# Optimization experiments

Hardware: AMD Instinct MI355X
Metric: run time of the kernel (lower is better)

## Reference

```python
import jax, jax.numpy as jnp
import numpy as np

# init hyperparameters (from init_kwargs)
KD = KH = KW = 3
SD = SH = SW = 1
PD = PH = PW = 1
DD = DH = DW = 1
GROUPS = 1
DG = 1  # deformable_groups
CIN, COUT = 32, 64


def setup_inputs() -> dict:
    key = jax.random.key(0)
    k1, k2, k3, k4, k5 = jax.random.split(key, 5)
    B, D, H, W = 2, 8, 48, 48
    K = KD * KH * KW
    x = jax.random.normal(k1, (B, CIN, D, H, W), dtype=jnp.float32)
    # 2 offset components (h, w) per deformable-group kernel tap
    offset = jax.random.normal(k2, (B, 2 * DG * K, D, H, W), dtype=jnp.float32)
    mask = jax.random.uniform(k3, (B, DG * K, D, H, W), dtype=jnp.float32)
    fan_in = CIN // GROUPS * K
    weight = jax.random.normal(k4, (COUT, CIN // GROUPS, KD, KH, KW), dtype=jnp.float32) / np.sqrt(fan_in)
    bias = jax.random.uniform(k5, (COUT,), dtype=jnp.float32, minval=-1.0, maxval=1.0) / np.sqrt(fan_in)
    return {"input": x, "offset": offset, "mask": mask, "weight": weight, "bias": bias}


def reference(input, offset, mask, weight, bias):
    x = input
    B, Cin, D, H, W = x.shape
    Cout = weight.shape[0]
    K = KD * KH * KW
    Do = (D + 2 * PD - DD * (KD - 1) - 1) // SD + 1
    Ho = (H + 2 * PH - DH * (KH - 1) - 1) // SH + 1
    Wo = (W + 2 * PW - DW * (KW - 1) - 1) // SW + 1
    Cg = Cin // DG

    kdi, khi, kwi = [a.reshape(-1) for a in jnp.meshgrid(
        jnp.arange(KD), jnp.arange(KH), jnp.arange(KW), indexing="ij")]
    # depth taps: regular (un-deformed) dilated grid -> exact integer index
    d_pos = kdi[:, None] * DD + jnp.arange(Do) * SD - PD           # [K, Do]
    valid_d = (d_pos >= 0) & (d_pos < D)
    d_idx = jnp.clip(d_pos, 0, D - 1)
    h_base = (khi[:, None] * DH + jnp.arange(Ho) * SH - PH).astype(x.dtype)  # [K, Ho]
    w_base = (kwi[:, None] * DW + jnp.arange(Wo) * SW - PW).astype(x.dtype)  # [K, Wo]

    off = offset.reshape(B, DG, K, 2, Do, Ho, Wo)
    m = mask.reshape(B, DG, K, Do, Ho, Wo)

    h = h_base[None, None, :, None, :, None] + off[:, :, :, 0]     # [B,DG,K,Do,Ho,Wo]
    w = w_base[None, None, :, None, None, :] + off[:, :, :, 1]
    h0f, w0f = jnp.floor(h), jnp.floor(w)
    lh, lw = h - h0f, w - w0f
    h0, w0 = h0f.astype(jnp.int32), w0f.astype(jnp.int32)
    h1, w1 = h0 + 1, w0 + 1

    vd = valid_d[None, None, :, :, None, None]
    inb_h = lambda hi: (hi >= 0) & (hi < H)
    inb_w = lambda wi: (wi >= 0) & (wi < W)

    xg = x.reshape(B, DG, Cg, D, H, W)

    def gather(hI, wI):
        hc = jnp.clip(hI, 0, H - 1)
        wc = jnp.clip(wI, 0, W - 1)
        def per(xi, hh, ww):  # xi [Cg,D,H,W]; hh,ww [K,Do,Ho,Wo]
            dfull = jnp.broadcast_to(d_idx[:, :, None, None], hh.shape)
            return xi[:, dfull, hh, ww]  # [Cg,K,Do,Ho,Wo]
        return jax.vmap(jax.vmap(per))(xg, hc, wc)  # [B,DG,Cg,K,Do,Ho,Wo]

    w00 = ((1 - lh) * (1 - lw) * (inb_h(h0) & inb_w(w0) & vd))[:, :, None]
    w01 = ((1 - lh) * lw * (inb_h(h0) & inb_w(w1) & vd))[:, :, None]
    w10 = (lh * (1 - lw) * (inb_h(h1) & inb_w(w0) & vd))[:, :, None]
    w11 = (lh * lw * (inb_h(h1) & inb_w(w1) & vd))[:, :, None]

    val = (gather(h0, w0) * w00 + gather(h0, w1) * w01 +
           gather(h1, w0) * w10 + gather(h1, w1) * w11)   # [B,DG,Cg,K,Do,Ho,Wo]

    sampled = (val * m[:, :, None]).reshape(B, Cin, K, Do, Ho, Wo)
    w2 = weight.reshape(Cout, Cin // GROUPS, K)  # groups == 1
    out = jnp.einsum("bckdhw,ock->bodhw", sampled, w2)
    return out + bias[None, :, None, None, None]
```

## Files before the change

kernel.cpp:

```cpp
#include <hip/hip_runtime.h>
#include <hip/hip_bf16.h>
#include <hip/hip_fp16.h>

#define BSZ 2
#define CIN 32
#define COUT 64
#define DD_ 8
#define HH_ 48
#define WW_ 48
#define KK 27
#define HWs (HH_*WW_)
#define DHW (DD_*HH_*WW_)
#define NT 768
#define NBLK (BSZ*DD_*HH_)

typedef __attribute__((ext_vector_type(8))) _Float16 half8;
typedef __attribute__((ext_vector_type(4))) float f32x4;

__global__ void prep(const float* __restrict__ x, const float* __restrict__ wsrc,
                     _Float16* __restrict__ xT, _Float16* __restrict__ wf) {
    __shared__ float tile[CIN][WW_];
    int blk = blockIdx.x;
    if (blk < NBLK) {
        int h = blk % HH_;
        int t0 = blk / HH_;
        int d = t0 % DD_;
        int b = t0 / DD_;
        int base = d * HWs + h * WW_;
        for (int e = threadIdx.x; e < CIN * WW_; e += 256) {
            int ci = e / WW_, w = e - ci * WW_;
            tile[ci][w] = x[(size_t)(b * CIN + ci) * DHW + base + w];
        }
        __syncthreads();
        for (int e = threadIdx.x; e < CIN * WW_; e += 256) {
            int w = e >> 5, ci = e & 31;
            xT[(size_t)(b * DHW + base + w) * CIN + ci] = (_Float16)tile[ci][w];
        }
    } else {
        int idx = (blk - NBLK) * 256 + threadIdx.x;
        if (idx < KK * 4 * 64 * 8) {
            int j = idx & 7, l = (idx >> 3) & 63, c = (idx >> 9) & 3, k = idx >> 11;
            int co = c * 16 + (l & 15), ci = (l >> 4) * 8 + j;
            wf[idx] = (_Float16)wsrc[(co * CIN + ci) * KK + k];
        }
    }
}

#define SPLAT8(H) {H, H, H, H, H, H, H, H}

template<int USE_XT>
__launch_bounds__(NT, 4)
__global__ void dcn3d(const float* __restrict__ x, const _Float16* __restrict__ xT,
                      const float* __restrict__ off, const float* __restrict__ msk,
                      const float* __restrict__ wsrc, const _Float16* __restrict__ wf,
                      const float* __restrict__ bias, float* __restrict__ out) {
    int blk = blockIdx.x;
    int h = blk % HH_;
    int t0 = blk / HH_;
    int d = t0 % DD_;
    int b = t0 / DD_;

    __shared__ half8 Sh[14 * 3 * 4 * 16];

    int tid = threadIdx.x;
    int lane = tid & 63;
    int wid = tid >> 6;
    int cstrip = wid & 3;
    int T = wid >> 2;
    int spb = d * HWs + h * WW_;

    const _Float16* xTb = xT + (size_t)b * DHW * CIN;
    const float* xb = x + (size_t)b * CIN * DHW;

#define PREP(HF, NK, KB)                                                        \
    int sp00_##HF = 0, sp01_##HF = 0, sp10_##HF = 0, sp11_##HF = 0;             \
    float f00_##HF = 0.f, f01_##HF = 0.f, f10_##HF = 0.f, f11_##HF = 0.f;       \
    if (tid < (NK) * 48) {                                                      \
        int kl = tid / 48;                                                      \
        int w = tid - kl * 48;                                                  \
        int k = (KB) + kl;                                                      \
        int kd = k / 9, kh2 = (k / 3) % 3, kw2 = k % 3;                         \
        int dpos = d + kd - 1;                                                  \
        bool vd = (dpos >= 0) && (dpos < DD_);                                  \
        int didx = min(max(dpos, 0), DD_ - 1);                                  \
        int rb = didx * HWs;                                                    \
        int sp = spb + w;                                                       \
        float oh = off[(b * (2 * KK) + 2 * k) * DHW + sp];                      \
        float ow = off[(b * (2 * KK) + 2 * k + 1) * DHW + sp];                  \
        float m  = msk[(b * KK + k) * DHW + sp];                                \
        float vm = vd ? m : 0.f;                                                \
        float hhf = (float)(kh2 + h - 1) + oh;                                  \
        float wwf = (float)(kw2 + w - 1) + ow;                                  \
        float h0f = floorf(hhf), w0f = floorf(wwf);                             \
        float lh = hhf - h0f, lw = wwf - w0f;                                   \
        int h0 = (int)h0f, w0 = (int)w0f, h1 = h0 + 1, w1 = w0 + 1;             \
        bool ih0 = (h0 >= 0) && (h0 < HH_), ih1 = (h1 >= 0) && (h1 < HH_);      \
        bool iw0 = (w0 >= 0) && (w0 < WW_), iw1 = (w1 >= 0) && (w1 < WW_);      \
        int h0c = min(max(h0, 0), HH_ - 1), h1c = min(max(h1, 0), HH_ - 1);     \
        int w0c = min(max(w0, 0), WW_ - 1), w1c = min(max(w1, 0), WW_ - 1);     \
        f00_##HF = (ih0 && iw0) ? (1.f - lh) * (1.f - lw) * vm : 0.f;           \
        f01_##HF = (ih0 && iw1) ? (1.f - lh) * lw * vm : 0.f;                   \
        f10_##HF = (ih1 && iw0) ? lh * (1.f - lw) * vm : 0.f;                   \
        f11_##HF = (ih1 && iw1) ? lh * lw * vm : 0.f;                           \
        sp00_##HF = rb + h0c * WW_ + w0c;                                       \
        sp01_##HF = rb + h0c * WW_ + w1c;                                       \
        sp10_##HF = rb + h1c * WW_ + w0c;                                       \
        sp11_##HF = rb + h1c * WW_ + w1c;                                       \
    }

    PREP(0, 14, 0)
    PREP(1, 13, 14)

#define SAMPLE(HF, NK)                                                          \
    if (tid < (NK) * 48) {                                                      \
        int kl = tid / 48;                                                      \
        int w = tid - kl * 48;                                                  \
        int sb = (kl * 3 + (w >> 4)) * 64 + (w & 15);                           \
        if (USE_XT) {                                                           \
            _Float16 e00 = (_Float16)f00_##HF, e01 = (_Float16)f01_##HF;        \
            _Float16 e10 = (_Float16)f10_##HF, e11 = (_Float16)f11_##HF;        \
            half8 v00 = SPLAT8(e00), v01 = SPLAT8(e01);                         \
            half8 v10 = SPLAT8(e10), v11 = SPLAT8(e11);                         \
            const half8* p00 = (const half8*)(xTb + ((size_t)sp00_##HF << 5));  \
            const half8* p01 = (const half8*)(xTb + ((size_t)sp01_##HF << 5));  \
            const half8* p10 = (const half8*)(xTb + ((size_t)sp10_##HF << 5));  \
            const half8* p11 = (const half8*)(xTb + ((size_t)sp11_##HF << 5));  \
            _Pragma("unroll")                                                   \
            for (int g = 0; g < 4; ++g)                                         \
                Sh[sb + g * 16] = p00[g] * v00 + p01[g] * v01                   \
                                + p10[g] * v10 + p11[g] * v11;                  \
        } else {                                                                \
            _Pragma("unroll")                                                   \
            for (int g = 0; g < 4; ++g) {                                       \
                half8 cv;                                                       \
                _Pragma("unroll")                                               \
                for (int j = 0; j < 8; ++j) {                                   \
                    const float* xp = xb + (size_t)(g * 8 + j) * DHW;           \
                    float v = f00_##HF * xp[sp00_##HF] + f01_##HF * xp[sp01_##HF] \
                            + f10_##HF * xp[sp10_##HF] + f11_##HF * xp[sp11_##HF]; \
                    cv[j] = (_Float16)v;                                        \
                }                                                               \
                Sh[sb + g * 16] = cv;                                           \
            }                                                                   \
        }                                                                       \
    }

    f32x4 acc = {0.f, 0.f, 0.f, 0.f};

#define GEMM(NK, KB)                                                            \
    _Pragma("unroll 7")                                                         \
    for (int kl = 0; kl < (NK); ++kl) {                                         \
        half8 a;                                                                \
        if (USE_XT) {                                                           \
            a = *(const half8*)(wf + ((((KB) + kl) * 4 + cstrip) * 64 + lane) * 8); \
        } else {                                                                \
            int co = cstrip * 16 + (lane & 15);                                 \
            int ci0 = (lane >> 4) * 8;                                          \
            _Pragma("unroll")                                                   \
            for (int j = 0; j < 8; ++j)                                         \
                a[j] = (_Float16)wsrc[(co * CIN + ci0 + j) * KK + (KB) + kl];   \
        }                                                                       \
        half8 bf = Sh[(kl * 3 + T) * 64 + (lane >> 4) * 16 + (lane & 15)];      \
        acc = __builtin_amdgcn_mfma_f32_16x16x32_f16(a, bf, acc, 0, 0, 0);      \
    }

    SAMPLE(0, 14)
    __syncthreads();
    GEMM(14, 0)
    __syncthreads();
    SAMPLE(1, 13)
    __syncthreads();
    GEMM(13, 14)

    int co0 = cstrip * 16 + (lane >> 4) * 4;
    int wcol = T * 16 + (lane & 15);
#pragma unroll
    for (int r = 0; r < 4; ++r)
        out[((b * COUT + co0 + r) * DD_ + d) * HWs + h * WW_ + wcol] = acc[r] + bias[co0 + r];

#undef PREP
#undef SAMPLE
#undef GEMM
}

extern "C" void kernel_launch(void* const* d_in, const int* in_sizes, int n_in,
                              void* d_out, int out_size, void* d_ws, size_t ws_size,
                              hipStream_t stream) {
    const float* x    = (const float*)d_in[0];
    const float* off  = (const float*)d_in[1];
    const float* msk  = (const float*)d_in[2];
    const float* w    = (const float*)d_in[3];
    const float* bias = (const float*)d_in[4];
    float* out = (float*)d_out;

    const size_t WF_BYTES = (size_t)KK * 4 * 64 * 8 * sizeof(_Float16);
    const size_t XT_OFF   = 131072;
    const size_t XT_BYTES = (size_t)BSZ * DHW * CIN * sizeof(_Float16);

    _Float16* wf = (_Float16*)d_ws;
    _Float16* xT = (_Float16*)((char*)d_ws + XT_OFF);
    int use = (ws_size >= XT_OFF + XT_BYTES && WF_BYTES <= XT_OFF) ? 1 : 0;

    if (use) {
        int wblocks = (KK * 4 * 64 * 8 + 255) / 256;
        prep<<<NBLK + wblocks, 256, 0, stream>>>(x, w, xT, wf);
        dcn3d<1><<<NBLK, NT, 0, stream>>>(x, xT, off, msk, w, wf, bias, out);
    } else {
        dcn3d<0><<<NBLK, NT, 0, stream>>>(x, xT, off, msk, w, wf, bias, out);
    }
}
```

Measured before the change: 43.50 us.

## Split kernel taps across three blocks with atomic accumulation into bias-initialized output

The main kernel now launches three times as many blocks, each covering a group of 9 of the 27 kernel taps for one output row. Partial results are combined with atomicAdd into an output buffer that a new kernel pre-fills with bias. The sampling loop is also rebalanced so each thread handles one 8-channel slice instead of all four, and the launch bound is raised to 6 blocks per CU. This is meant to increase parallelism and occupancy, at the cost of an extra launch, atomic traffic on the output, and a nondeterministic summation order.

```diff
diff --git a/kernel.cpp b/kernel.cpp
--- a/kernel.cpp
+++ b/kernel.cpp
@@ -1,5 +1,4 @@
 #include <hip/hip_runtime.h>
-#include <hip/hip_bf16.h>
 #include <hip/hip_fp16.h>
 
 #define BSZ 2
@@ -11,11 +10,21 @@
 #define KK 27
 #define HWs (HH_*WW_)
 #define DHW (DD_*HH_*WW_)
+#define NBLK (BSZ*DD_*HH_)
+#define KG 9
 #define NT 768
-#define NBLK (BSZ*DD_*HH_)
 
 typedef __attribute__((ext_vector_type(8))) _Float16 half8;
 typedef __attribute__((ext_vector_type(4))) float f32x4;
+
+__global__ void init_out(const float* __restrict__ bias, float* __restrict__ out) {
+    int o4 = blockIdx.x * 256 + threadIdx.x;
+    if (o4 >= BSZ * COUT * DHW / 4) return;
+    int o = o4 * 4;
+    float bv = bias[(o / DHW) & (COUT - 1)];
+    float4 v = {bv, bv, bv, bv};
+    *(float4*)(out + o) = v;
+}
 
 __global__ void prep(const float* __restrict__ x, const float* __restrict__ wsrc,
                      _Float16* __restrict__ xT, _Float16* __restrict__ wf) {
@@ -46,141 +55,119 @@
     }
 }
 
-#define SPLAT8(H) {H, H, H, H, H, H, H, H}
-
 template<int USE_XT>
-__launch_bounds__(NT, 4)
+__launch_bounds__(NT, 6)
 __global__ void dcn3d(const float* __restrict__ x, const _Float16* __restrict__ xT,
                       const float* __restrict__ off, const float* __restrict__ msk,
                       const float* __restrict__ wsrc, const _Float16* __restrict__ wf,
-                      const float* __restrict__ bias, float* __restrict__ out) {
+                      float* __restrict__ out) {
     int blk = blockIdx.x;
-    int h = blk % HH_;
-    int t0 = blk / HH_;
+    int kg  = blk / NBLK;
+    int row = blk - kg * NBLK;
+    int h = row % HH_;
+    int t0 = row / HH_;
     int d = t0 % DD_;
     int b = t0 / DD_;
 
-    __shared__ half8 Sh[14 * 3 * 4 * 16];
+    __shared__ half8 Sh[KG * 3 * 64];
 
     int tid = threadIdx.x;
     int lane = tid & 63;
     int wid = tid >> 6;
-    int cstrip = wid & 3;
-    int T = wid >> 2;
     int spb = d * HWs + h * WW_;
 
     const _Float16* xTb = xT + (size_t)b * DHW * CIN;
     const float* xb = x + (size_t)b * CIN * DHW;
 
-#define PREP(HF, NK, KB)                                                        \
-    int sp00_##HF = 0, sp01_##HF = 0, sp10_##HF = 0, sp11_##HF = 0;             \
-    float f00_##HF = 0.f, f01_##HF = 0.f, f10_##HF = 0.f, f11_##HF = 0.f;       \
-    if (tid < (NK) * 48) {                                                      \
-        int kl = tid / 48;                                                      \
-        int w = tid - kl * 48;                                                  \
-        int k = (KB) + kl;                                                      \
-        int kd = k / 9, kh2 = (k / 3) % 3, kw2 = k % 3;                         \
-        int dpos = d + kd - 1;                                                  \
-        bool vd = (dpos >= 0) && (dpos < DD_);                                  \
-        int didx = min(max(dpos, 0), DD_ - 1);                                  \
-        int rb = didx * HWs;                                                    \
-        int sp = spb + w;                                                       \
-        float oh = off[(b * (2 * KK) + 2 * k) * DHW + sp];                      \
-        float ow = off[(b * (2 * KK) + 2 * k + 1) * DHW + sp];                  \
-        float m  = msk[(b * KK + k) * DHW + sp];                                \
-        float vm = vd ? m : 0.f;                                                \
-        float hhf = (float)(kh2 + h - 1) + oh;                                  \
-        float wwf = (float)(kw2 + w - 1) + ow;                                  \
-        float h0f = floorf(hhf), w0f = floorf(wwf);                             \
-        float lh = hhf - h0f, lw = wwf - w0f;                                   \
-        int h0 = (int)h0f, w0 = (int)w0f, h1 = h0 + 1, w1 = w0 + 1;             \
-        bool ih0 = (h0 >= 0) && (h0 < HH_), ih1 = (h1 >= 0) && (h1 < HH_);      \
-        bool iw0 = (w0 >= 0) && (w0 < WW_), iw1 = (w1 >= 0) && (w1 < WW_);      \
-        int h0c = min(max(h0, 0), HH_ - 1), h1c = min(max(h1, 0), HH_ - 1);     \
-        int w0c = min(max(w0, 0), WW_ - 1), w1c = min(max(w1, 0), WW_ - 1);     \
-        f00_##HF = (ih0 && iw0) ? (1.f - lh) * (1.f - lw) * vm : 0.f;           \
-        f01_##HF = (ih0 && iw1) ? (1.f - lh) * lw * vm : 0.f;                   \
-        f10_##HF = (ih1 && iw0) ? lh * (1.f - lw) * vm : 0.f;                   \
-        f11_##HF = (ih1 && iw1) ? lh * lw * vm : 0.f;                           \
-        sp00_##HF = rb + h0c * WW_ + w0c;                                       \
-        sp01_##HF = rb + h0c * WW_ + w1c;                                       \
-        sp10_##HF = rb + h1c * WW_ + w0c;                                       \
-        sp11_##HF = rb + h1c * WW_ + w1c;                                       \
+#pragma unroll
+    for (int i = 0; i < 3; ++i) {
+        int t = tid + i * NT;
+        if (t < KG * 48 * 4) {
+            int p = t >> 2, g = t & 3;
+            int kl = p / 48;
+            int w  = p - kl * 48;
+            int k  = kg * KG + kl;
+            int kd = k / 9, kh2 = (k / 3) % 3, kw2 = k % 3;
+            int dpos = d + kd - 1;
+            bool vd = (dpos >= 0) && (dpos < DD_);
+            int didx = min(max(dpos, 0), DD_ - 1);
+            int rb = didx * HWs;
+            int sp = spb + w;
+            float oh = off[(b * (2 * KK) + 2 * k) * DHW + sp];
+            float ow = off[(b * (2 * KK) + 2 * k + 1) * DHW + sp];
+            float m  = msk[(b * KK + k) * DHW + sp];
+            float vm = vd ? m : 0.f;
+            float hhf = (float)(kh2 + h - 1) + oh;
+            float wwf = (float)(kw2 + w - 1) + ow;
+            float h0f = floorf(hhf), w0f = floorf(wwf);
+            float lh = hhf - h0f, lw = wwf - w0f;
+            int h0 = (int)h0f, w0 = (int)w0f, h1 = h0 + 1, w1 = w0 + 1;
+            bool ih0 = (h0 >= 0) && (h0 < HH_), ih1 = (h1 >= 0) && (h1 < HH_);
+            bool iw0 = (w0 >= 0) && (w0 < WW_), iw1 = (w1 >= 0) && (w1 < WW_);
+            int h0c = min(max(h0, 0), HH_ - 1), h1c = min(max(h1, 0), HH_ - 1);
+            int w0c = min(max(w0, 0), WW_ - 1), w1c = min(max(w1, 0), WW_ - 1);
+            float f00 = (ih0 && iw0) ? (1.f - lh) * (1.f - lw) * vm : 0.f;
+            float f01 = (ih0 && iw1) ? (1.f - lh) * lw * vm : 0.f;
+            float f10 = (ih1 && iw0) ? lh * (1.f - lw) * vm : 0.f;
+            float f11 = (ih1 && iw1) ? lh * lw * vm : 0.f;
+            int sp00 = rb + h0c * WW_ + w0c;
+            int sp01 = rb + h0c * WW_ + w1c;
+            int sp10 = rb + h1c * WW_ + w0c;
+            int sp11 = rb + h1c * WW_ + w1c;
+            int sb = (kl * 3 + (w >> 4)) * 64 + g * 16 + (w & 15);
+            if (USE_XT) {
+                const _Float16* bp = xTb + g * 8;
+                half8 c00 = *(const half8*)(bp + ((size_t)sp00 << 5));
+                half8 c01 = *(const half8*)(bp + ((size_t)sp01 << 5));
+                half8 c10 = *(const half8*)(bp + ((size_t)sp10 << 5));
+                half8 c11 = *(const half8*)(bp + ((size_t)sp11 << 5));
+                _Float16 e00 = (_Float16)f00, e01 = (_Float16)f01;
+                _Float16 e10 = (_Float16)f10, e11 = (_Float16)f11;
+                half8 v00 = {e00,e00,e00,e00,e00,e00,e00,e00};
+                half8 v01 = {e01,e01,e01,e01,e01,e01,e01,e01};
+                half8 v10 = {e10,e10,e10,e10,e10,e10,e10,e10};
+                half8 v11 = {e11,e11,e11,e11,e11,e11,e11,e11};
+                Sh[sb] = c00 * v00 + c01 * v01 + c10 * v10 + c11 * v11;
+            } else {
+                half8 cv;
+#pragma unroll
+                for (int j = 0; j < 8; ++j) {
+                    const float* xp = xb + (size_t)(g * 8 + j) * DHW;
+                    float v = f00 * xp[sp00] + f01 * xp[sp01]
+                            + f10 * xp[sp10] + f11 * xp[sp11];
+                    cv[j] = (_Float16)v;
+                }
+                Sh[sb] = cv;
+            }
+        }
     }
+    __syncthreads();
 
-    PREP(0, 14, 0)
-    PREP(1, 13, 14)
-
-#define SAMPLE(HF, NK)                                                          \
-    if (tid < (NK) * 48) {                                                      \
-        int kl = tid / 48;                                                      \
-        int w = tid - kl * 48;                                                  \
-        int sb = (kl * 3 + (w >> 4)) * 64 + (w & 15);                           \
-        if (USE_XT) {                                                           \
-            _Float16 e00 = (_Float16)f00_##HF, e01 = (_Float16)f01_##HF;        \
-            _Float16 e10 = (_Float16)f10_##HF, e11 = (_Float16)f11_##HF;        \
-            half8 v00 = SPLAT8(e00), v01 = SPLAT8(e01);                         \
-            half8 v10 = SPLAT8(e10), v11 = SPLAT8(e11);                         \
-            const half8* p00 = (const half8*)(xTb + ((size_t)sp00_##HF << 5));  \
-            const half8* p01 = (const half8*)(xTb + ((size_t)sp01_##HF << 5));  \
-            const half8* p10 = (const half8*)(xTb + ((size_t)sp10_##HF << 5));  \
-            const half8* p11 = (const half8*)(xTb + ((size_t)sp11_##HF << 5));  \
-            _Pragma("unroll")                                                   \
-            for (int g = 0; g < 4; ++g)                                         \
-                Sh[sb + g * 16] = p00[g] * v00 + p01[g] * v01                   \
-                                + p10[g] * v10 + p11[g] * v11;                  \
-        } else {                                                                \
-            _Pragma("unroll")                                                   \
-            for (int g = 0; g < 4; ++g) {                                       \
-                half8 cv;                                                       \
-                _Pragma("unroll")                                               \
-                for (int j = 0; j < 8; ++j) {                                   \
-                    const float* xp = xb + (size_t)(g * 8 + j) * DHW;           \
-                    float v = f00_##HF * xp[sp00_##HF] + f01_##HF * xp[sp01_##HF] \
-                            + f10_##HF * xp[sp10_##HF] + f11_##HF * xp[sp11_##HF]; \
-                    cv[j] = (_Float16)v;                                        \
-                }                                                               \
-                Sh[sb + g * 16] = cv;                                           \
-            }                                                                   \
-        }                                                                       \
+    int cstrip = wid & 3;
+    int T = wid >> 2;
+    f32x4 acc = {0.f, 0.f, 0.f, 0.f};
+#pragma unroll
+    for (int kl = 0; kl < KG; ++kl) {
+        int k = kg * KG + kl;
+        half8 a;
+        if (USE_XT) {
+            a = *(const half8*)(wf + ((k * 4 + cstrip) * 64 + lane) * 8);
+        } else {
+            int co = cstrip * 16 + (lane & 15);
+            int ci0 = (lane >> 4) * 8;
+#pragma unroll
+            for (int j = 0; j < 8; ++j)
+                a[j] = (_Float16)wsrc[(co * CIN + ci0 + j) * KK + k];
+        }
+        half8 bfr = Sh[(kl * 3 + T) * 64 + (lane >> 4) * 16 + (lane & 15)];
+        acc = __builtin_amdgcn_mfma_f32_16x16x32_f16(a, bfr, acc, 0, 0, 0);
     }
-
-    f32x4 acc = {0.f, 0.f, 0.f, 0.f};
-
-#define GEMM(NK, KB)                                                            \
-    _Pragma("unroll 7")                                                         \
-    for (int kl = 0; kl < (NK); ++kl) {                                         \
-        half8 a;                                                                \
-        if (USE_XT) {                                                           \
-            a = *(const half8*)(wf + ((((KB) + kl) * 4 + cstrip) * 64 + lane) * 8); \
-        } else {                                                                \
-            int co = cstrip * 16 + (lane & 15);                                 \
-            int ci0 = (lane >> 4) * 8;                                          \
-            _Pragma("unroll")                                                   \
-            for (int j = 0; j < 8; ++j)                                         \
-                a[j] = (_Float16)wsrc[(co * CIN + ci0 + j) * KK + (KB) + kl];   \
-        }                                                                       \
-        half8 bf = Sh[(kl * 3 + T) * 64 + (lane >> 4) * 16 + (lane & 15)];      \
-        acc = __builtin_amdgcn_mfma_f32_16x16x32_f16(a, bf, acc, 0, 0, 0);      \
-    }
-
-    SAMPLE(0, 14)
-    __syncthreads();
-    GEMM(14, 0)
-    __syncthreads();
-    SAMPLE(1, 13)
-    __syncthreads();
-    GEMM(13, 14)
 
     int co0 = cstrip * 16 + (lane >> 4) * 4;
     int wcol = T * 16 + (lane & 15);
 #pragma unroll
     for (int r = 0; r < 4; ++r)
-        out[((b * COUT + co0 + r) * DD_ + d) * HWs + h * WW_ + wcol] = acc[r] + bias[co0 + r];
-
-#undef PREP
-#undef SAMPLE
-#undef GEMM
+        atomicAdd(&out[((b * COUT + co0 + r) * DD_ + d) * HWs + h * WW_ + wcol], acc[r]);
 }
 
 extern "C" void kernel_launch(void* const* d_in, const int* in_sizes, int n_in,
@@ -199,13 +186,14 @@
 
     _Float16* wf = (_Float16*)d_ws;
     _Float16* xT = (_Float16*)((char*)d_ws + XT_OFF);
-    int use = (ws_size >= XT_OFF + XT_BYTES && WF_BYTES <= XT_OFF) ? 1 : 0;
+    int use = (ws_size >= XT_OFF + XT_BYTES) ? 1 : 0;
 
+    init_out<<<(BSZ * COUT * DHW / 4 + 255) / 256, 256, 0, stream>>>(bias, out);
     if (use) {
         int wblocks = (KK * 4 * 64 * 8 + 255) / 256;
         prep<<<NBLK + wblocks, 256, 0, stream>>>(x, w, xT, wf);
-        dcn3d<1><<<NBLK, NT, 0, stream>>>(x, xT, off, msk, w, wf, bias, out);
+        dcn3d<1><<<3 * NBLK, NT, 0, stream>>>(x, xT, off, msk, w, wf, out);
     } else {
-        dcn3d<0><<<NBLK, NT, 0, stream>>>(x, xT, off, msk, w, wf, bias, out);
+        dcn3d<0><<<3 * NBLK, NT, 0, stream>>>(x, xT, off, msk, w, wf, out);
     }
 }
```

New measurement: 48.65 us. +11.8%, slower.
